# Kernel optimization log

Hardware: AMD Instinct MI355X
Metric: run time of the kernel (lower is better)

Reference implementation:

```python
import jax, jax.numpy as jnp
import numpy as np

HEAD, D_MODEL, D_KV = 16, 1024, 64
B, NQ, NK = 2, 2048, 2048


def setup_inputs() -> dict:
    key = jax.random.key(0)
    ks = jax.random.split(key, 10)
    s = 1.0 / np.sqrt(D_MODEL)
    return {
        "queries": jax.random.normal(ks[0], (B, NQ, D_MODEL), jnp.float32),
        "keys": jax.random.normal(ks[1], (B, NK, D_MODEL), jnp.float32),
        "values": jax.random.normal(ks[2], (B, NK, D_MODEL), jnp.float32),
        "group_prob": jax.random.uniform(ks[3], (B, 1, NQ, NK), jnp.float32),
        "attention_mask": jnp.ones((B, NK), jnp.int32),
        "Wq": jax.random.normal(ks[4], (D_MODEL, HEAD * D_KV), jnp.float32) * s,
        "bq": jnp.zeros((HEAD * D_KV,), jnp.float32),
        "Wk": jax.random.normal(ks[5], (D_MODEL, HEAD * D_KV), jnp.float32) * s,
        "bk": jnp.zeros((HEAD * D_KV,), jnp.float32),
        "Wv": jax.random.normal(ks[6], (D_MODEL, HEAD * D_KV), jnp.float32) * s,
        "bv": jnp.zeros((HEAD * D_KV,), jnp.float32),
    }


def reference(queries, keys, values, group_prob, attention_mask, Wq, bq, Wk, bk, Wv, bv):
    b_s, nq, _ = queries.shape
    nk = keys.shape[1]
    # projections -> [b, h, n, d]
    q = (queries @ Wq + bq).reshape(b_s, nq, HEAD, D_KV).transpose(0, 2, 1, 3)
    k = (keys @ Wk + bk).reshape(b_s, nk, HEAD, D_KV).transpose(0, 2, 1, 3)
    v = (values @ Wv + bv).reshape(b_s, nk, HEAD, D_KV).transpose(0, 2, 1, 3)
    att = jnp.einsum("bhqd,bhkd->bhqk", q, k) / np.sqrt(D_KV).astype(np.float32)
    # NOTE: original uses non-in-place `att.masked_fill(...)` and discards the
    # result, so attention_mask has NO effect on the computation. Replicated.
    att = jax.nn.softmax(att, axis=-1)
    att = att * group_prob  # post-softmax group gating, broadcast over heads
    out = jnp.einsum("bhqk,bhkd->bhqd", att, v)
    return out.transpose(0, 2, 1, 3).reshape(b_s, nq, D_MODEL)
```

## Files before the change

kernel.cpp:

```cpp
#include <hip/hip_runtime.h>
#include <hip/hip_bf16.h>
#include <cstdint>

typedef unsigned short ushort_t;
typedef __attribute__((ext_vector_type(8))) short short8;
typedef __attribute__((ext_vector_type(4))) float floatx4;

#define H_   16
#define DKV_ 64
#define DM_  1024
#define B_   2
#define NQ_  2048
#define NK_  2048

__device__ __forceinline__ unsigned short f2bf(float f) {
  union { float f; unsigned int u; } v; v.f = f;
  unsigned int u = v.u;
  return (unsigned short)((u + 0x7fffu + ((u >> 16) & 1u)) >> 16);
}

__device__ __forceinline__ float fexp2(float x) { return __builtin_amdgcn_exp2f(x); }
__device__ __forceinline__ float frcp(float x)  { return __builtin_amdgcn_rcpf(x); }

__device__ __forceinline__ floatx4 mfma16(short8 a, short8 b, floatx4 c) {
  return __builtin_amdgcn_mfma_f32_16x16x32_bf16(a, b, c, 0, 0, 0);
}

constexpr int LDT = 40;

__global__ __launch_bounds__(256, 2) void proj_kernel(
    const float* __restrict__ Xq, const float* __restrict__ Xk, const float* __restrict__ Xv,
    const float* __restrict__ Wq, const float* __restrict__ Wk, const float* __restrict__ Wv,
    const float* __restrict__ bq, const float* __restrict__ bk, const float* __restrict__ bv,
    ushort_t* __restrict__ Qb, ushort_t* __restrict__ Kb, ushort_t* __restrict__ Vt)
{
  const int mode = blockIdx.z;
  const float* X    = (mode == 0) ? Xq : (mode == 1) ? Xk : Xv;
  const float* W    = (mode == 0) ? Wq : (mode == 1) ? Wk : Wv;
  const float* bias = (mode == 0) ? bq : (mode == 1) ? bk : bv;
  ushort_t* dst     = (mode == 0) ? Qb : (mode == 1) ? Kb : Vt;

  __shared__ ushort_t Asm[128 * LDT];
  __shared__ ushort_t Bsm[128 * LDT];

  const int tid = threadIdx.x, lane = tid & 63, wid = tid >> 6;
  const int m0 = blockIdx.y * 128, n0 = blockIdx.x * 128;
  const int c = lane & 15, g = lane >> 4;
  const int wm = wid & 1, wn = wid >> 1, mb = wm * 64, nb = wn * 64;

  floatx4 acc[4][4];
  #pragma unroll
  for (int i = 0; i < 4; i++)
    #pragma unroll
    for (int j = 0; j < 4; j++) acc[i][j] = floatx4{0.f, 0.f, 0.f, 0.f};

  const int ar = tid >> 1, ah = tid & 1;
  const int bn = tid & 127, bh2 = tid >> 7;

  for (int k0 = 0; k0 < DM_; k0 += 32) {
    const floatx4* ap = (const floatx4*)(X + (size_t)(m0 + ar) * DM_ + k0 + ah * 16);
    floatx4 av0 = ap[0], av1 = ap[1], av2 = ap[2], av3 = ap[3];
    const float* wp = W + (size_t)(k0 + bh2 * 16) * 1024 + n0 + bn;
    float wv[16];
    #pragma unroll
    for (int j = 0; j < 16; j++) wv[j] = wp[j * 1024];

    short8 pa0, pa1, pb0, pb1;
    #pragma unroll
    for (int j = 0; j < 4; j++) {
      pa0[j] = (short)f2bf(av0[j]); pa0[4 + j] = (short)f2bf(av1[j]);
      pa1[j] = (short)f2bf(av2[j]); pa1[4 + j] = (short)f2bf(av3[j]);
    }
    #pragma unroll
    for (int j = 0; j < 8; j++) { pb0[j] = (short)f2bf(wv[j]); pb1[j] = (short)f2bf(wv[8 + j]); }

    __syncthreads();
    *(short8*)&Asm[ar * LDT + ah * 16]      = pa0;
    *(short8*)&Asm[ar * LDT + ah * 16 + 8]  = pa1;
    *(short8*)&Bsm[bn * LDT + bh2 * 16]     = pb0;
    *(short8*)&Bsm[bn * LDT + bh2 * 16 + 8] = pb1;
    __syncthreads();

    short8 af[4], bfr[4];
    #pragma unroll
    for (int i = 0; i < 4; i++) af[i]  = *(const short8*)&Asm[(mb + i * 16 + c) * LDT + g * 8];
    #pragma unroll
    for (int j = 0; j < 4; j++) bfr[j] = *(const short8*)&Bsm[(nb + j * 16 + c) * LDT + g * 8];
    #pragma unroll
    for (int i = 0; i < 4; i++)
      #pragma unroll
      for (int j = 0; j < 4; j++) acc[i][j] = mfma16(af[i], bfr[j], acc[i][j]);
  }

  #pragma unroll
  for (int j = 0; j < 4; j++) {
    const int col = n0 + nb + j * 16 + c;
    const float bv_ = bias[col];
    const int h = col >> 6, d = col & 63;
    #pragma unroll
    for (int i = 0; i < 4; i++) {
      #pragma unroll
      for (int r = 0; r < 4; r++) {
        const int row = m0 + mb + i * 16 + g * 4 + r;
        const int b = row >> 11, n = row & 2047;
        float v = acc[i][j][r] + bv_;
        if (mode == 0) {
          v *= 0.18033688011112042f;
          dst[((size_t)(b * H_ + h) * NQ_ + n) * DKV_ + d] = f2bf(v);
        } else if (mode == 1) {
          dst[((size_t)(b * H_ + h) * NQ_ + n) * DKV_ + d] = f2bf(v);
        } else {
          dst[((size_t)(b * H_ + h) * DKV_ + d) * NK_ + n] = f2bf(v);
        }
      }
    }
  }
}

__global__ __launch_bounds__(256, 2) void attn_kernel(
    const ushort_t* __restrict__ Qb, const ushort_t* __restrict__ Kb,
    const ushort_t* __restrict__ Vt, const float* __restrict__ gp,
    float* __restrict__ out)
{
  __shared__ ushort_t Ks[2][64 * 72];
  __shared__ ushort_t Vs[2][64 * 72];
  __shared__ ushort_t Pl[4][32 * 72];

  const int tid = threadIdx.x, lane = tid & 63, wid = tid >> 6;
  const int c = lane & 15, g = lane >> 4;
  const int h = blockIdx.x, b = blockIdx.z;
  const int bh = b * H_ + h;
  const int qw = blockIdx.y * 128 + wid * 32;

  const ushort_t* Qp = Qb + (size_t)bh * NQ_ * DKV_;
  const ushort_t* Kp = Kb + (size_t)bh * NK_ * DKV_;
  const ushort_t* Vp = Vt + (size_t)bh * DKV_ * NK_;
  const float* gpp = gp + (size_t)b * NQ_ * NK_ + (size_t)qw * NK_;
  ushort_t* Pw = Pl[wid];

  const int srow = wid * 16 + (lane >> 2);
  const int scol = (lane & 3) * 8;

  short8 qf[2][2];
  #pragma unroll
  for (int i = 0; i < 2; i++)
    #pragma unroll
    for (int kc = 0; kc < 2; kc++)
      qf[i][kc] = *(const short8*)&Qp[(qw + i * 16 + c) * DKV_ + kc * 32 + g * 8];

  #pragma unroll
  for (int half = 0; half < 2; half++) {
    short8 kv = *(const short8*)&Kp[(size_t)srow * DKV_ + scol + half * 32];
    short8 vv = *(const short8*)&Vp[(size_t)srow * NK_ + scol + half * 32];
    *(short8*)&Ks[0][srow * 72 + scol + half * 32] = kv;
    *(short8*)&Vs[0][srow * 72 + scol + half * 32] = vv;
  }
  __syncthreads();

  floatx4 o[2][4];
  float l[2][4];
  #pragma unroll
  for (int i = 0; i < 2; i++) {
    #pragma unroll
    for (int jd = 0; jd < 4; jd++) o[i][jd] = floatx4{0.f, 0.f, 0.f, 0.f};
    #pragma unroll
    for (int r = 0; r < 4; r++) l[i][r] = 0.f;
  }

  for (int t = 0; t < NK_ / 64; t++) {
    const int k0 = t * 64;
    const int cur = t & 1, nxt = cur ^ 1;

    float gpv[2][4][4];
    #pragma unroll
    for (int i = 0; i < 2; i++)
      #pragma unroll
      for (int r = 0; r < 4; r++) {
        const float* gq = gpp + (size_t)(i * 16 + g * 4 + r) * NK_ + k0 + c;
        #pragma unroll
        for (int jk = 0; jk < 4; jk++) gpv[i][jk][r] = gq[jk * 16];
      }

    short8 knx[2], vnx[2];
    const bool has_next = (t + 1) < NK_ / 64;
    if (has_next) {
      const int k1 = k0 + 64;
      #pragma unroll
      for (int half = 0; half < 2; half++) {
        knx[half] = *(const short8*)&Kp[(size_t)(k1 + srow) * DKV_ + scol + half * 32];
        vnx[half] = *(const short8*)&Vp[(size_t)srow * NK_ + k1 + scol + half * 32];
      }
    }

    floatx4 s[2][4];
    #pragma unroll
    for (int i = 0; i < 2; i++)
      #pragma unroll
      for (int jk = 0; jk < 4; jk++) s[i][jk] = floatx4{0.f, 0.f, 0.f, 0.f};
    #pragma unroll
    for (int jk = 0; jk < 4; jk++) {
      #pragma unroll
      for (int kc = 0; kc < 2; kc++) {
        short8 kf = *(const short8*)&Ks[cur][(jk * 16 + c) * 72 + kc * 32 + g * 8];
        #pragma unroll
        for (int i = 0; i < 2; i++) s[i][jk] = mfma16(qf[i][kc], kf, s[i][jk]);
      }
    }

    #pragma unroll
    for (int i = 0; i < 2; i++)
      #pragma unroll
      for (int jk = 0; jk < 4; jk++)
        #pragma unroll
        for (int r = 0; r < 4; r++) {
          const float p = fexp2(s[i][jk][r]);
          l[i][r] += p;
          Pw[(i * 16 + g * 4 + r) * 72 + jk * 16 + c] = f2bf(p * gpv[i][jk][r]);
        }

    #pragma unroll
    for (int kc = 0; kc < 2; kc++) {
      short8 af0 = *(const short8*)&Pw[(0 * 16 + c) * 72 + kc * 32 + g * 8];
      short8 af1 = *(const short8*)&Pw[(1 * 16 + c) * 72 + kc * 32 + g * 8];
      #pragma unroll
      for (int jd = 0; jd < 4; jd++) {
        short8 vf = *(const short8*)&Vs[cur][(jd * 16 + c) * 72 + kc * 32 + g * 8];
        o[0][jd] = mfma16(af0, vf, o[0][jd]);
        o[1][jd] = mfma16(af1, vf, o[1][jd]);
      }
    }

    if (has_next) {
      #pragma unroll
      for (int half = 0; half < 2; half++) {
        *(short8*)&Ks[nxt][srow * 72 + scol + half * 32] = knx[half];
        *(short8*)&Vs[nxt][srow * 72 + scol + half * 32] = vnx[half];
      }
    }
    __syncthreads();
  }

  float invl[2][4];
  #pragma unroll
  for (int i = 0; i < 2; i++)
    #pragma unroll
    for (int r = 0; r < 4; r++) {
      float rs = l[i][r];
      rs += __shfl_xor(rs, 1);
      rs += __shfl_xor(rs, 2);
      rs += __shfl_xor(rs, 4);
      rs += __shfl_xor(rs, 8);
      invl[i][r] = frcp(rs);
    }
  #pragma unroll
  for (int i = 0; i < 2; i++)
    #pragma unroll
    for (int jd = 0; jd < 4; jd++)
      #pragma unroll
      for (int r = 0; r < 4; r++) {
        const int row = qw + i * 16 + g * 4 + r;
        out[(size_t)(b * NQ_ + row) * 1024 + h * 64 + jd * 16 + c] =
            o[i][jd][r] * invl[i][r];
      }
}

extern "C" void kernel_launch(void* const* d_in, const int* in_sizes, int n_in,
                              void* d_out, int out_size, void* d_ws, size_t ws_size,
                              hipStream_t stream) {
  const float* queries = (const float*)d_in[0];
  const float* keys    = (const float*)d_in[1];
  const float* values  = (const float*)d_in[2];
  const float* gp      = (const float*)d_in[3];
  const float* Wq = (const float*)d_in[5];
  const float* bq = (const float*)d_in[6];
  const float* Wk = (const float*)d_in[7];
  const float* bk = (const float*)d_in[8];
  const float* Wv = (const float*)d_in[9];
  const float* bv = (const float*)d_in[10];

  ushort_t* Qb = (ushort_t*)d_ws;
  ushort_t* Kb = Qb + (size_t)B_ * H_ * NQ_ * DKV_;
  ushort_t* Vt = Kb + (size_t)B_ * H_ * NK_ * DKV_;
  float* out = (float*)d_out;

  proj_kernel<<<dim3(8, 32, 3), 256, 0, stream>>>(
      queries, keys, values, Wq, Wk, Wv, bq, bk, bv, Qb, Kb, Vt);
  attn_kernel<<<dim3(H_, NQ_ / 128, B_), 256, 0, stream>>>(Qb, Kb, Vt, gp, out);
}
```

Baseline: 275.6 us.

## Pre-cast inputs and weights to bf16, use direct global-to-LDS loads in projection

Adds separate kernels that cast X to bf16 and cast plus transpose W to bf16, so the projection GEMM can load bf16 tiles straight into LDS with global_load_lds instead of doing strided fp32 loads and in-loop conversion. The projection epilogue now stages results through LDS to issue vectorized coalesced stores, including for the transposed V layout. It costs two extra launches and extra workspace traffic for the bf16 copies. If the workspace is too small it falls back to the old kernel.

Result: faster. 252.9 us (-8.2%).

```diff
diff --git a/kernel.cpp b/kernel.cpp
--- a/kernel.cpp
+++ b/kernel.cpp
@@ -5,6 +5,7 @@
 typedef unsigned short ushort_t;
 typedef __attribute__((ext_vector_type(8))) short short8;
 typedef __attribute__((ext_vector_type(4))) float floatx4;
+typedef __attribute__((ext_vector_type(4))) unsigned short ushort4_t;
 
 #define H_   16
 #define DKV_ 64
@@ -26,9 +27,154 @@
   return __builtin_amdgcn_mfma_f32_16x16x32_bf16(a, b, c, 0, 0, 0);
 }
 
+__device__ __forceinline__ void gload_lds16(const ushort_t* g, ushort_t* l) {
+  __builtin_amdgcn_global_load_lds(
+      (const __attribute__((address_space(1))) void*)g,
+      (__attribute__((address_space(3))) void*)l, 16, 0, 0);
+}
+
+__global__ __launch_bounds__(256) void cast_x_kernel(
+    const float* __restrict__ q, const float* __restrict__ k,
+    const float* __restrict__ v, ushort_t* __restrict__ dst)
+{
+  const int t = blockIdx.y;
+  const float* src = (t == 0) ? q : (t == 1) ? k : v;
+  ushort_t* d = dst + (size_t)t * 4096 * 1024;
+  const int gid = blockIdx.x * 256 + threadIdx.x;
+  #pragma unroll
+  for (int u = 0; u < 8; u++) {
+    const int i4 = u * 131072 + gid;
+    floatx4 f = ((const floatx4*)src)[i4];
+    ushort4_t o;
+    #pragma unroll
+    for (int e = 0; e < 4; e++) o[e] = f2bf(f[e]);
+    *(ushort4_t*)&d[(size_t)i4 * 4] = o;
+  }
+}
+
+__global__ __launch_bounds__(256) void cast_wt_kernel(
+    const float* __restrict__ Wq, const float* __restrict__ Wk,
+    const float* __restrict__ Wv, ushort_t* __restrict__ WtAll)
+{
+  __shared__ ushort_t tile[32][33];
+  const int t = blockIdx.z;
+  const float* W = (t == 0) ? Wq : (t == 1) ? Wk : Wv;
+  ushort_t* Wt = WtAll + (size_t)t * 1024 * 1024;
+  const int n0 = blockIdx.x * 32, k0 = blockIdx.y * 32;
+  const int tid = threadIdx.x, r = tid >> 3, c4 = (tid & 7) * 4;
+  floatx4 f = *(const floatx4*)&W[(size_t)(k0 + r) * 1024 + n0 + c4];
+  #pragma unroll
+  for (int e = 0; e < 4; e++) tile[r][c4 + e] = f2bf(f[e]);
+  __syncthreads();
+  ushort4_t o;
+  #pragma unroll
+  for (int e = 0; e < 4; e++) o[e] = tile[c4 + e][r];
+  *(ushort4_t*)&Wt[(size_t)(n0 + r) * 1024 + k0 + c4] = o;
+}
+
+__global__ __launch_bounds__(256, 2) void proj_kernel2(
+    const ushort_t* __restrict__ Xbf, const ushort_t* __restrict__ WtAll,
+    const float* __restrict__ bq, const float* __restrict__ bk,
+    const float* __restrict__ bv,
+    ushort_t* __restrict__ Qb, ushort_t* __restrict__ Kb, ushort_t* __restrict__ Vt)
+{
+  const int mode = blockIdx.z;
+  const ushort_t* X  = Xbf  + (size_t)mode * 4096 * 1024;
+  const ushort_t* Wt = WtAll + (size_t)mode * 1024 * 1024;
+  const float* bias  = (mode == 0) ? bq : (mode == 1) ? bk : bv;
+  ushort_t* dst      = (mode == 0) ? Qb : (mode == 1) ? Kb : Vt;
+
+  __shared__ ushort_t SM[8192];
+  ushort_t* SA = SM;
+  ushort_t* SB = SM + 4096;
+
+  const int tid = threadIdx.x, lane = tid & 63, wid = tid >> 6;
+  const int c = lane & 15, g = lane >> 4;
+  const int m0 = blockIdx.y * 128, n0 = blockIdx.x * 128;
+  const int wm = wid & 1, wn = wid >> 1, mb = wm * 64, nb = wn * 64;
+  const int srow = lane >> 2;
+  const int schunk = (lane & 3) * 8;
+
+  floatx4 acc[4][4];
+  #pragma unroll
+  for (int i = 0; i < 4; i++)
+    #pragma unroll
+    for (int j = 0; j < 4; j++) acc[i][j] = floatx4{0.f, 0.f, 0.f, 0.f};
+
+  for (int k0 = 0; k0 < DM_; k0 += 32) {
+    __syncthreads();
+    #pragma unroll
+    for (int u = 0; u < 2; u++) {
+      const int t = wid * 2 + u;
+      gload_lds16(&X [(size_t)(m0 + t * 16 + srow) * 1024 + k0 + schunk], &SA[t * 512]);
+      gload_lds16(&Wt[(size_t)(n0 + t * 16 + srow) * 1024 + k0 + schunk], &SB[t * 512]);
+    }
+    __syncthreads();
+
+    short8 af[4], bfr[4];
+    #pragma unroll
+    for (int i = 0; i < 4; i++) af[i]  = *(const short8*)&SA[(mb + i * 16 + c) * 32 + g * 8];
+    #pragma unroll
+    for (int j = 0; j < 4; j++) bfr[j] = *(const short8*)&SB[(nb + j * 16 + c) * 32 + g * 8];
+    #pragma unroll
+    for (int i = 0; i < 4; i++)
+      #pragma unroll
+      for (int j = 0; j < 4; j++) acc[i][j] = mfma16(af[i], bfr[j], acc[i][j]);
+  }
+
+  __syncthreads();
+  const float scale = (mode == 0) ? 0.18033688011112042f : 1.0f;
+  ushort_t* EP = SM + wid * 2048;
+  const int hh = (n0 + nb) >> 6;
+
+  if (mode != 2) {
+    for (int jj = 0; jj < 2; jj++) {
+      #pragma unroll
+      for (int jt = 0; jt < 2; jt++) {
+        const int j = jj * 2 + jt;
+        const float bb = bias[n0 + nb + j * 16 + c];
+        #pragma unroll
+        for (int i = 0; i < 4; i++)
+          #pragma unroll
+          for (int r = 0; r < 4; r++)
+            EP[(i * 16 + g * 4 + r) * 32 + jt * 16 + c] =
+                f2bf((acc[i][j][r] + bb) * scale);
+      }
+      #pragma unroll
+      for (int u = 0; u < 8; u++) {
+        const int rowl = u * 8 + (lane >> 3);
+        ushort4_t vv = *(ushort4_t*)&EP[rowl * 32 + (lane & 7) * 4];
+        const int rowg = m0 + mb + rowl;
+        const int bb2 = rowg >> 11, nn = rowg & 2047;
+        *(ushort4_t*)&dst[((size_t)(bb2 * H_ + hh) * NQ_ + nn) * DKV_ +
+                          jj * 32 + (lane & 7) * 4] = vv;
+      }
+    }
+  } else {
+    const int bb2 = (m0 + mb) >> 11, nloc = (m0 + mb) & 2047;
+    for (int j = 0; j < 4; j++) {
+      const float bb = bias[n0 + nb + j * 16 + c];
+      #pragma unroll
+      for (int i = 0; i < 4; i++) {
+        ushort4_t pk;
+        #pragma unroll
+        for (int r = 0; r < 4; r++) pk[r] = f2bf(acc[i][j][r] + bb);
+        *(ushort4_t*)&EP[c * 72 + i * 16 + g * 4] = pk;
+      }
+      const int d0 = j * 16;
+      #pragma unroll
+      for (int u = 0; u < 2; u++) {
+        const int coll = u * 8 + (lane >> 3);
+        short8 vv = *(const short8*)&EP[coll * 72 + (lane & 7) * 8];
+        *(short8*)&dst[((size_t)(bb2 * H_ + hh) * DKV_ + d0 + coll) * NK_ +
+                       nloc + (lane & 7) * 8] = vv;
+      }
+    }
+  }
+}
+
 constexpr int LDT = 40;
-
-__global__ __launch_bounds__(256, 2) void proj_kernel(
+__global__ __launch_bounds__(256, 2) void proj_kernel_fb(
     const float* __restrict__ Xq, const float* __restrict__ Xk, const float* __restrict__ Xv,
     const float* __restrict__ Wq, const float* __restrict__ Wk, const float* __restrict__ Wv,
     const float* __restrict__ bq, const float* __restrict__ bk, const float* __restrict__ bv,
@@ -64,7 +210,6 @@
     float wv[16];
     #pragma unroll
     for (int j = 0; j < 16; j++) wv[j] = wp[j * 1024];
-
     short8 pa0, pa1, pb0, pb1;
     #pragma unroll
     for (int j = 0; j < 4; j++) {
@@ -73,14 +218,12 @@
     }
     #pragma unroll
     for (int j = 0; j < 8; j++) { pb0[j] = (short)f2bf(wv[j]); pb1[j] = (short)f2bf(wv[8 + j]); }
-
     __syncthreads();
     *(short8*)&Asm[ar * LDT + ah * 16]      = pa0;
     *(short8*)&Asm[ar * LDT + ah * 16 + 8]  = pa1;
     *(short8*)&Bsm[bn * LDT + bh2 * 16]     = pb0;
     *(short8*)&Bsm[bn * LDT + bh2 * 16 + 8] = pb1;
     __syncthreads();
-
     short8 af[4], bfr[4];
     #pragma unroll
     for (int i = 0; i < 4; i++) af[i]  = *(const short8*)&Asm[(mb + i * 16 + c) * LDT + g * 8];
@@ -91,14 +234,13 @@
       #pragma unroll
       for (int j = 0; j < 4; j++) acc[i][j] = mfma16(af[i], bfr[j], acc[i][j]);
   }
-
   #pragma unroll
   for (int j = 0; j < 4; j++) {
     const int col = n0 + nb + j * 16 + c;
     const float bv_ = bias[col];
     const int h = col >> 6, d = col & 63;
     #pragma unroll
-    for (int i = 0; i < 4; i++) {
+    for (int i = 0; i < 4; i++)
       #pragma unroll
       for (int r = 0; r < 4; r++) {
         const int row = m0 + mb + i * 16 + g * 4 + r;
@@ -113,7 +255,6 @@
           dst[((size_t)(b * H_ + h) * DKV_ + d) * NK_ + n] = f2bf(v);
         }
       }
-    }
   }
 }
 
@@ -278,12 +419,26 @@
   const float* Wv = (const float*)d_in[9];
   const float* bv = (const float*)d_in[10];
 
+  const size_t SZ_QKV = (size_t)3 * B_ * H_ * NQ_ * DKV_;
+  const size_t SZ_X   = (size_t)3 * 4096 * 1024;
+  const size_t SZ_W   = (size_t)3 * 1024 * 1024;
+  const size_t NEED   = (SZ_QKV + SZ_X + SZ_W) * sizeof(ushort_t);
+
   ushort_t* Qb = (ushort_t*)d_ws;
   ushort_t* Kb = Qb + (size_t)B_ * H_ * NQ_ * DKV_;
   ushort_t* Vt = Kb + (size_t)B_ * H_ * NK_ * DKV_;
   float* out = (float*)d_out;
 
-  proj_kernel<<<dim3(8, 32, 3), 256, 0, stream>>>(
-      queries, keys, values, Wq, Wk, Wv, bq, bk, bv, Qb, Kb, Vt);
+  if (ws_size >= NEED) {
+    ushort_t* Xbf = Qb + SZ_QKV;
+    ushort_t* Wt  = Xbf + SZ_X;
+    cast_x_kernel<<<dim3(512, 3), 256, 0, stream>>>(queries, keys, values, Xbf);
+    cast_wt_kernel<<<dim3(32, 32, 3), 256, 0, stream>>>(Wq, Wk, Wv, Wt);
+    proj_kernel2<<<dim3(8, 32, 3), 256, 0, stream>>>(
+        Xbf, Wt, bq, bk, bv, Qb, Kb, Vt);
+  } else {
+    proj_kernel_fb<<<dim3(8, 32, 3), 256, 0, stream>>>(
+        queries, keys, values, Wq, Wk, Wv, bq, bk, bv, Qb, Kb, Vt);
+  }
   attn_kernel<<<dim3(H_, NQ_ / 128, B_), 256, 0, stream>>>(Qb, Kb, Vt, gp, out);
 }
```
